# Optimization experiments

Measured on AMD Instinct MI355X. Metric: run time of the kernel, lower is better.

Reference implementation:

```python
import jax, jax.numpy as jnp
import numpy as np

N_M, N_D, N_A = 100000, 30000, 80000


def setup_inputs() -> dict:
    key = jax.random.key(0)
    ks = jax.random.split(key, 24)
    d_in, d_h, d_out = 64, 64, 32
    inp = {
        "x_movie": jax.random.normal(ks[0], (N_M, d_in), jnp.float32),
        "x_director": jax.random.normal(ks[1], (N_D, d_in), jnp.float32),
        "x_actor": jax.random.normal(ks[2], (N_A, d_in), jnp.float32),
        "src_md": jax.random.randint(ks[3], (1500000,), 0, N_M, jnp.int32),
        "dst_md": jax.random.randint(ks[4], (1500000,), 0, N_D, jnp.int32),
        "ew_md": jax.random.uniform(ks[5], (1500000,), jnp.float32),
        "src_dm": jax.random.randint(ks[6], (1500000,), 0, N_D, jnp.int32),
        "dst_dm": jax.random.randint(ks[7], (1500000,), 0, N_M, jnp.int32),
        "ew_dm": jax.random.uniform(ks[8], (1500000,), jnp.float32),
        "src_ma": jax.random.randint(ks[9], (2000000,), 0, N_M, jnp.int32),
        "dst_ma": jax.random.randint(ks[10], (2000000,), 0, N_A, jnp.int32),
        "ew_ma": jax.random.uniform(ks[11], (2000000,), jnp.float32),
        "src_am": jax.random.randint(ks[12], (2000000,), 0, N_A, jnp.int32),
        "dst_am": jax.random.randint(ks[13], (2000000,), 0, N_M, jnp.int32),
        "ew_am": jax.random.uniform(ks[14], (2000000,), jnp.float32),
        "W1_rel": jax.random.normal(ks[15], (4, d_in, d_h), jnp.float32) * 0.05,
        "b1": jax.random.normal(ks[16], (4, d_h), jnp.float32) * 0.05,
        "W1_root": jax.random.normal(ks[17], (4, d_in, d_h), jnp.float32) * 0.05,
        "W2_rel": jax.random.normal(ks[18], (4, d_h, d_out), jnp.float32) * 0.05,
        "b2": jax.random.normal(ks[19], (4, d_out), jnp.float32) * 0.05,
        "W2_root": jax.random.normal(ks[20], (4, d_h, d_out), jnp.float32) * 0.05,
    }
    return inp


def _hetero_layer(x_m, x_d, x_a, edges, ews, W_rel, b, W_root):
    # relation order: 0 = movie->director, 1 = director->movie,
    #                 2 = movie->actor,    3 = actor->movie
    (src_md, dst_md, src_dm, dst_dm, src_ma, dst_ma, src_am, dst_am) = edges
    (ew_md, ew_dm, ew_ma, ew_am) = ews
    # GraphConv: aggregate edge-weighted source features, then linear.
    agg_md = jax.ops.segment_sum(x_m[src_md] * ew_md[:, None], dst_md, num_segments=N_D)
    agg_dm = jax.ops.segment_sum(x_d[src_dm] * ew_dm[:, None], dst_dm, num_segments=N_M)
    agg_ma = jax.ops.segment_sum(x_m[src_ma] * ew_ma[:, None], dst_ma, num_segments=N_A)
    agg_am = jax.ops.segment_sum(x_a[src_am] * ew_am[:, None], dst_am, num_segments=N_M)
    out_d = agg_md @ W_rel[0] + b[0] + x_d @ W_root[0]
    out_m = (agg_dm @ W_rel[1] + b[1] + x_m @ W_root[1]) \
          + (agg_am @ W_rel[3] + b[3] + x_m @ W_root[3])  # HeteroConv aggr='sum'
    out_a = agg_ma @ W_rel[2] + b[2] + x_a @ W_root[2]
    return out_m, out_d, out_a


def reference(x_movie, x_director, x_actor,
              src_md, dst_md, ew_md, src_dm, dst_dm, ew_dm,
              src_ma, dst_ma, ew_ma, src_am, dst_am, ew_am,
              W1_rel, b1, W1_root, W2_rel, b2, W2_root):
    edges = (src_md, dst_md, src_dm, dst_dm, src_ma, dst_ma, src_am, dst_am)
    ews = (ew_md, ew_dm, ew_ma, ew_am)
    h_m, h_d, h_a = _hetero_layer(x_movie, x_director, x_actor, edges, ews, W1_rel, b1, W1_root)
    h_m, h_d, h_a = jax.nn.relu(h_m), jax.nn.relu(h_d), jax.nn.relu(h_a)
    o_m, o_d, o_a = _hetero_layer(h_m, h_d, h_a, edges, ews, W2_rel, b2, W2_root)
    return o_m, o_d, o_a
```

## Files before the change

### kernel.cpp

```cpp
#include <hip/hip_runtime.h>

#define N_M 100000
#define N_D 30000
#define N_A 80000

#define CSHIFT 14
#define NC_M 7
#define NC_D 2
#define NC_A 5

#define BO_MD 0
#define BO_DM (BO_MD + N_D * NC_M)
#define BO_MA (BO_DM + N_M * NC_D)
#define BO_AM (BO_MA + N_A * NC_M)
#define B_TOT (BO_AM + N_M * NC_A)

#define FBITS 12
#define NFINE 4096
#define NBUCK ((B_TOT + NFINE - 1) / NFINE)
#define T_A 4096

typedef unsigned int u32;
typedef unsigned short u16;
typedef unsigned long long u64;
// ... 150 lines not shown
    int gb = binBase0 + f0 + i;
    if (gb < B_TOT) bins[gb] = s0 + (int)ex;
    cur2[f0 + i] = ex;
    ex += v[i];
  }
  if (c == NBUCK - 1 && tid == 0) bins[B_TOT] = s1;
  __syncthreads();
  for (int e = s0 + tid; e < s1; e += 256) {
    u64 t = tmp[e];
    u32 fine = (u32)(t >> 32) & (NFINE - 1);
    u32 pos = atomicAdd(&cur2[fine], 1u);
    pairs[s0 + pos] = (u32)t;
  }
}

__global__ __launch_bounds__(256) void l1_tr_m(
    const float* __restrict__ x,
    const float* __restrict__ Wr0, const float* __restrict__ Wr2,
    const float* __restrict__ Wt1, const float* __restrict__ Wt3,
    const float* __restrict__ b1a, const float* __restrict__ b1b,
    u16* __restrict__ t0, u16* __restrict__ t2, u16* __restrict__ r, int n) {
  __shared__ float A[4096], B[4096], C[4096];
  for (int i = threadIdx.x * 4; i < 4096; i += 1024) {
    *(float4*)&A[i] = *(const float4*)&Wr0[i];
    *(float4*)&B[i] = *(const float4*)&Wr2[i];
    float4 p = *(const float4*)&Wt1[i], q = *(const float4*)&Wt3[i];
    *(float4*)&C[i] = make_float4(p.x + q.x, p.y + q.y, p.z + q.z, p.w + q.w);
  }
  __syncthreads();
  int lane = threadIdx.x & 63, wid = threadIdx.x >> 6;
  int wave = blockIdx.x * 4 + wid, nW = gridDim.x * 4;
  float bj = b1a[lane] + b1b[lane];
  for (int base = wave * 4; base < n; base += nW * 4) {
    int n0 = base, n1 = min(base + 1, n - 1), n2 = min(base + 2, n - 1), n3 = min(base + 3, n - 1);
    float o0a = 0, o0b = 0, o0c = bj, o1a = 0, o1b = 0, o1c = bj;
    float o2a = 0, o2b = 0, o2c = bj, o3a = 0, o3b = 0, o3c = bj;
#pragma unroll 4
    for (int k = 0; k < 64; k++) {
      float wa = A[k * 64 + lane], wb = B[k * 64 + lane], wc = C[k * 64 + lane];
      float x0 = x[(size_t)n0 * 64 + k], x1 = x[(size_t)n1 * 64 + k];
      float x2 = x[(size_t)n2 * 64 + k], x3 = x[(size_t)n3 * 64 + k];
      o0a = fmaf(x0, wa, o0a); o0b = fmaf(x0, wb, o0b); o0c = fmaf(x0, wc, o0c);
      o1a = fmaf(x1, wa, o1a); o1b = fmaf(x1, wb, o1b); o1c = fmaf(x1, wc, o1c);
      o2a = fmaf(x2, wa, o2a); o2b = fmaf(x2, wb, o2b); o2c = fmaf(x2, wc, o2c);
      o3a = fmaf(x3, wa, o3a); o3b = fmaf(x3, wb, o3b); o3c = fmaf(x3, wc, o3c);
    }
    t0[(size_t)n0 * 64 + lane] = f2bf(o0a); t2[(size_t)n0 * 64 + lane] = f2bf(o0b); r[(size_t)n0 * 64 + lane] = f2bf(o0c);
    if (base + 1 < n) { t0[(size_t)n1 * 64 + lane] = f2bf(o1a); t2[(size_t)n1 * 64 + lane] = f2bf(o1b); r[(size_t)n1 * 64 + lane] = f2bf(o1c); }
    if (base + 2 < n) { t0[(size_t)n2 * 64 + lane] = f2bf(o2a); t2[(size_t)n2 * 64 + lane] = f2bf(o2b); r[(size_t)n2 * 64 + lane] = f2bf(o2c); }
    if (base + 3 < n) { t0[(size_t)n3 * 64 + lane] = f2bf(o3a); t2[(size_t)n3 * 64 + lane] = f2bf(o3b); r[(size_t)n3 * 64 + lane] = f2bf(o3c); }
  }
}

__global__ __launch_bounds__(256) void l1_tr_s(
    const float* __restrict__ x,
    const float* __restrict__ Wrel, const float* __restrict__ Wroot,
    const float* __restrict__ bias,
    u16* __restrict__ t, u16* __restrict__ r, int n) {
  __shared__ float A[4096], C[4096];
  for (int i = threadIdx.x * 4; i < 4096; i += 1024) {
    *(float4*)&A[i] = *(const float4*)&Wrel[i];
    *(float4*)&C[i] = *(const float4*)&Wroot[i];
  }
  __syncthreads();
  int lane = threadIdx.x & 63, wid = threadIdx.x >> 6;
  int wave = blockIdx.x * 4 + wid, nW = gridDim.x * 4;
  float bj = bias[lane];
  for (int base = wave * 4; base < n; base += nW * 4) {
    int n0 = base, n1 = min(base + 1, n - 1), n2 = min(base + 2, n - 1), n3 = min(base + 3, n - 1);
    float o0a = 0, o0c = bj, o1a = 0, o1c = bj, o2a = 0, o2c = bj, o3a = 0, o3c = bj;
#pragma unroll 4
    for (int k = 0; k < 64; k++) {
      float wa = A[k * 64 + lane], wc = C[k * 64 + lane];
      float x0 = x[(size_t)n0 * 64 + k], x1 = x[(size_t)n1 * 64 + k];
      float x2 = x[(size_t)n2 * 64 + k], x3 = x[(size_t)n3 * 64 + k];
      o0a = fmaf(x0, wa, o0a); o0c = fmaf(x0, wc, o0c);
      o1a = fmaf(x1, wa, o1a); o1c = fmaf(x1, wc, o1c);
      o2a = fmaf(x2, wa, o2a); o2c = fmaf(x2, wc, o2c);
      o3a = fmaf(x3, wa, o3a); o3c = fmaf(x3, wc, o3c);
    }
    t[(size_t)n0 * 64 + lane] = f2bf(o0a); r[(size_t)n0 * 64 + lane] = f2bf(o0c);
    if (base + 1 < n) { t[(size_t)n1 * 64 + lane] = f2bf(o1a); r[(size_t)n1 * 64 + lane] = f2bf(o1c); }
    if (base + 2 < n) { t[(size_t)n2 * 64 + lane] = f2bf(o2a); r[(size_t)n2 * 64 + lane] = f2bf(o2c); }
    if (base + 3 < n) { t[(size_t)n3 * 64 + lane] = f2bf(o3a); r[(size_t)n3 * 64 + lane] = f2bf(o3c); }
  }
}

__device__ __forceinline__ void gather2_seg64(
    int s0, int s1, const u32* __restrict__ pairs,
    const u16* __restrict__ tbl, u32 lanebyte, u32 hm, int lane,
    float& a0, float& a1) {
  for (int base = s0; base < s1; base += 64) {
    int cnt = s1 - base; if (cnt > 64) cnt = 64;
    u32 pw = 0;
    if (base + lane < s1) pw = pairs[base + lane];
    int e = 0;
    for (; e + 4 <= cnt; e += 4) {
      u32 pa0 = __builtin_amdgcn_readlane(pw, e);
      u32 pb0 = __builtin_amdgcn_readlane(pw, e + 1);
      u32 pa1 = __builtin_amdgcn_readlane(pw, e + 2);
      u32 pb1 = __builtin_amdgcn_readlane(pw, e + 3);
      u32 offa0 = (pa0 >> 15) << 7;
      u32 offd0 = ((pb0 >> 15) << 7) - offa0;
      u32 wa0 = (pa0 & 0x7FFFu) << 16;
      u32 wd0 = (((pb0 & 0x7FFFu) << 16)) ^ wa0;
      u32 offa1 = (pa1 >> 15) << 7;
      u32 offd1 = ((pb1 >> 15) << 7) - offa1;
      u32 wa1 = (pa1 & 0x7FFFu) << 16;
      u32 wd1 = (((pb1 & 0x7FFFu) << 16)) ^ wa1;
      u32 off0 = (hm & offd0) + offa0 + lanebyte;
      u32 off1 = (hm & offd1) + offa1 + lanebyte;
      u32 v0 = *(const u32*)((const char*)tbl + off0);
      u32 v1 = *(const u32*)((const char*)tbl + off1);
      float w0 = __uint_as_float((hm & wd0) ^ wa0);
      float w1 = __uint_as_float((hm & wd1) ^ wa1);
      a0 = fmaf(w0, bf2f((u16)v0), a0);
      a1 = fmaf(w0, bf2f_hi(v0), a1);
      a0 = fmaf(w1, bf2f((u16)v1), a0);
      a1 = fmaf(w1, bf2f_hi(v1), a1);
    }
    if (e + 2 <= cnt) {
      u32 pa = __builtin_amdgcn_readlane(pw, e);
      u32 pb = __builtin_amdgcn_readlane(pw, e + 1);
      u32 offa = (pa >> 15) << 7;
      u32 offd = ((pb >> 15) << 7) - offa;
      u32 wa = (pa & 0x7FFFu) << 16;
      u32 wd = (((pb & 0x7FFFu) << 16)) ^ wa;
      u32 off = (hm & offd) + offa + lanebyte;
      u32 v = *(const u32*)((const char*)tbl + off);
      float w = __uint_as_float((hm & wd) ^ wa);
      a0 = fmaf(w, bf2f((u16)v), a0);
      a1 = fmaf(w, bf2f_hi(v), a1);
      e += 2;
    }
    if (e < cnt) {
      u32 p = __builtin_amdgcn_readlane(pw, e);
      u32 offa = (p >> 15) << 7;
      u32 wa = (p & 0x7FFFu) << 16;
      u32 off = offa + lanebyte;
      u32 v = *(const u32*)((const char*)tbl + off);
      float w = __uint_as_float((hm & wa) ^ wa);
      a0 = fmaf(w, bf2f((u16)v), a0);
      a1 = fmaf(w, bf2f_hi(v), a1);
    }
  }
}

__device__ __forceinline__ void gathero_32(
    int s0, int s1, const u32* __restrict__ pairs,
    const u16* __restrict__ ytbl, int lanebyte, int oaddr, int lane,
    float& a0, float& a1, float& a2, float& a3) {
  for (int base = s0; base < s1; base += 64) {
    u32 pw = 0;
    if (base + lane < s1) pw = pairs[base + lane];
    int ng = min(s1 - base, 64);
    ng = (ng + 7) >> 3;
#pragma unroll 2
    for (int g = 0; g < ng; g++) {
      u32 p = (u32)__builtin_amdgcn_ds_bpermute(oaddr + (g << 5), (int)pw);
      u32 off = ((p >> 15) << 6) + lanebyte;
      float w = __uint_as_float((p & 0x7FFFu) << 16);
      uint2 v = *(const uint2*)((const char*)ytbl + off);
      a0 = fmaf(w, bf2f((u16)v.x), a0);
      a1 = fmaf(w, bf2f_hi(v.x), a1);
      a2 = fmaf(w, bf2f((u16)v.y), a2);
      a3 = fmaf(w, bf2f_hi(v.y), a3);
    }
  }
}

__global__ __launch_bounds__(512) void fused1(
    const int* __restrict__ bins, const u32* __restrict__ pairs,
    const u16* __restrict__ tbl, const u16* __restrict__ r1,
    const float* __restrict__ W2r, const float* __restrict__ W2t,
    const float* __restrict__ b2s,
    u16* __restrict__ y, float* __restrict__ oroot,
    int n, int nC, int binBase) {
  __shared__ float Wy[2048], Wt[2048];
  __shared__ float bs[32];
  __shared__ __align__(16) float scr[8][64];
  for (int i = threadIdx.x; i < 2048; i += 512) { Wy[i] = W2r[i]; Wt[i] = W2t[i]; }
  if (threadIdx.x < 32) bs[threadIdx.x] = b2s[threadIdx.x];
  __syncthreads();
  int lane = threadIdx.x & 63, wid = threadIdx.x >> 6;
  int j = lane & 31, half = lane >> 5;
  u32 lanebyte = (u32)j << 2;
  u32 hm = half ? 0xFFFFFFFFu : 0u;
  int node0 = (blockIdx.x * 8 + wid) * 8;
  int bnd = bins[binBase + (node0 + min(lane, 8)) * nC];
  float acc0[8], acc1[8];
#pragma unroll
  for (int i = 0; i < 8; i++) { acc0[i] = 0.f; acc1[i] = 0.f; }
#pragma unroll
  for (int i = 0; i < 8; i++) {
    int s0 = __builtin_amdgcn_readlane(bnd, i);
    int s1 = __builtin_amdgcn_readlane(bnd, i + 1);
    if (node0 + i < n) gather2_seg64(s0, s1, pairs, tbl, lanebyte, hm, lane, acc0[i], acc1[i]);
  }
#pragma unroll
  for (int i = 0; i < 8; i++) {
    int node = node0 + i;
    if (node >= n) continue;
    float a0 = acc0[i] + __shfl_xor(acc0[i], 32);
    float a1 = acc1[i] + __shfl_xor(acc1[i], 32);
    u32 rv = *(const u32*)&r1[(size_t)node * 64 + 2 * j];
    float hv0 = fmaxf(a0 + bf2f((u16)rv), 0.f);
    float hv1 = fmaxf(a1 + bf2f_hi(rv), 0.f);
    if (!half) *(float2*)&scr[wid][2 * j] = make_float2(hv0, hv1);
    float oy = 0.f, ot = 0.f;
#pragma unroll
    for (int kk = 0; kk < 32; kk++) {
      int k = (half << 5) + kk;
      float s = scr[wid][k];
      oy = fmaf(s, Wy[k * 32 + j], oy);
      ot = fmaf(s, Wt[k * 32 + j], ot);
    }
    oy += __shfl_xor(oy, 32);
    ot += __shfl_xor(ot, 32);
    if (lane < 32) {
      y[(size_t)node * 32 + lane] = f2bf(oy);
      oroot[(size_t)node * 32 + lane] = ot + bs[lane];
    }
  }
}

__global__ __launch_bounds__(512) void fusedm(
    const int* __restrict__ bins, const u32* __restrict__ pairs,
    const u16* __restrict__ tbl1,
    const u16* __restrict__ tbl2,
    const u16* __restrict__ r1,
    const float* __restrict__ W2r0, const float* __restrict__ W2r2,
    const float* __restrict__ W2t1, const float* __restrict__ W2t3,
    const float* __restrict__ b2a, const float* __restrict__ b2b,
    u16* __restrict__ y0, u16* __restrict__ y2, float* __restrict__ oroot, int n) {
  __shared__ float Wy0[2048], Wy2[2048], Wt[2048];
  __shared__ float bs[32];
  __shared__ __align__(16) float scr[8][64];
  for (int i = threadIdx.x; i < 2048; i += 512) {
    Wy0[i] = W2r0[i]; Wy2[i] = W2r2[i]; Wt[i] = W2t1[i] + W2t3[i];
  }
  if (threadIdx.x < 32) bs[threadIdx.x] = b2a[threadIdx.x] + b2b[threadIdx.x];
  __syncthreads();
  int lane = threadIdx.x & 63, wid = threadIdx.x >> 6;
  int j = lane & 31, half = lane >> 5;
  u32 lanebyte = (u32)j << 2;
  u32 hm = half ? 0xFFFFFFFFu : 0u;
  int node0 = (blockIdx.x * 8 + wid) * 8;
  int bdm = bins[BO_DM + (node0 + min(lane, 8)) * NC_D];
  int bam = bins[BO_AM + (node0 + min(lane, 8)) * NC_A];
  float acc0[8], acc1[8];
#pragma unroll
  for (int i = 0; i < 8; i++) { acc0[i] = 0.f; acc1[i] = 0.f; }
#pragma unroll
  for (int i = 0; i < 8; i++) {
    int s0 = __builtin_amdgcn_readlane(bdm, i);
    int s1 = __builtin_amdgcn_readlane(bdm, i + 1);
    if (node0 + i < n) gather2_seg64(s0, s1, pairs, tbl1, lanebyte, hm, lane, acc0[i], acc1[i]);
  }
#pragma unroll
  for (int i = 0; i < 8; i++) {
    int s0 = __builtin_amdgcn_readlane(bam, i);
    int s1 = __builtin_amdgcn_readlane(bam, i + 1);
    if (node0 + i < n) gather2_seg64(s0, s1, pairs, tbl2, lanebyte, hm, lane, acc0[i], acc1[i]);
  }
#pragma unroll
  for (int i = 0; i < 8; i++) {
    int node = node0 + i;
    if (node >= n) continue;
    float a0 = acc0[i] + __shfl_xor(acc0[i], 32);
    float a1 = acc1[i] + __shfl_xor(acc1[i], 32);
    u32 rv = *(const u32*)&r1[(size_t)node * 64 + 2 * j];
    float hv0 = fmaxf(a0 + bf2f((u16)rv), 0.f);
    float hv1 = fmaxf(a1 + bf2f_hi(rv), 0.f);
    if (!half) *(float2*)&scr[wid][2 * j] = make_float2(hv0, hv1);
    float o0 = 0.f, o2 = 0.f, ot = 0.f;
#pragma unroll
    for (int kk = 0; kk < 32; kk++) {
      int k = (half << 5) + kk;
      float s = scr[wid][k];
      o0 = fmaf(s, Wy0[k * 32 + j], o0);
      o2 = fmaf(s, Wy2[k * 32 + j], o2);
      ot = fmaf(s, Wt[k * 32 + j], ot);
    }
    o0 += __shfl_xor(o0, 32);
    o2 += __shfl_xor(o2, 32);
    ot += __shfl_xor(ot, 32);
    if (lane < 32) {
      y0[(size_t)node * 32 + lane] = f2bf(o0);
      y2[(size_t)node * 32 + lane] = f2bf(o2);
      oroot[(size_t)node * 32 + lane] = ot + bs[lane];
    }
  }
}

__global__ __launch_bounds__(256) void out1(
    const int* __restrict__ bins, const u32* __restrict__ pairs,
    const u16* __restrict__ ytbl, float* __restrict__ out,
    int n, int nC, int binBase) {
  int lane = threadIdx.x & 63, wid = threadIdx.x >> 6;
  int node0 = (blockIdx.x * 4 + wid) * 8;
  int j8 = lane & 7;
  int lanebyte = j8 << 3;
  int oaddr = (lane >> 3) << 2;
  int bnd = bins[binBase + (node0 + min(lane, 8)) * nC];
  float acc0[8], acc1[8], acc2[8], acc3[8];
#pragma unroll
  for (int i = 0; i < 8; i++) { acc0[i] = 0.f; acc1[i] = 0.f; acc2[i] = 0.f; acc3[i] = 0.f; }
#pragma unroll
  for (int i = 0; i < 8; i++) {
    int s0 = __builtin_amdgcn_readlane(bnd, i);
    int s1 = __builtin_amdgcn_readlane(bnd, i + 1);
    if (node0 + i < n) gathero_32(s0, s1, pairs, ytbl, lanebyte, oaddr, lane,
                                  acc0[i], acc1[i], acc2[i], acc3[i]);
  }
#pragma unroll
  for (int i = 0; i < 8; i++) {
    int node = node0 + i;
    if (node >= n) continue;
    float a0 = acc0[i], a1 = acc1[i], a2 = acc2[i], a3 = acc3[i];
    a0 += __shfl_xor(a0, 8); a0 += __shfl_xor(a0, 16); a0 += __shfl_xor(a0, 32);
    a1 += __shfl_xor(a1, 8); a1 += __shfl_xor(a1, 16); a1 += __shfl_xor(a1, 32);
    a2 += __shfl_xor(a2, 8); a2 += __shfl_xor(a2, 16); a2 += __shfl_xor(a2, 32);
    a3 += __shfl_xor(a3, 8); a3 += __shfl_xor(a3, 16); a3 += __shfl_xor(a3, 32);
    if (lane < 8) {
      float4* o = (float4*)((char*)out + (size_t)node * 128 + (j8 << 4));
      float4 v = *o;
      v.x += a0; v.y += a1; v.z += a2; v.w += a3;
      *o = v;
    }
  }
}

__global__ __launch_bounds__(256) void outm(
    const int* __restrict__ bins, const u32* __restrict__ pairs,
    const u16* __restrict__ y1,
    const u16* __restrict__ y2,
    float* __restrict__ out, int n) {
  int lane = threadIdx.x & 63, wid = threadIdx.x >> 6;
  int node0 = (blockIdx.x * 4 + wid) * 8;
  int j8 = lane & 7;
  int lanebyte = j8 << 3;
  int oaddr = (lane >> 3) << 2;
  int bdm = bins[BO_DM + (node0 + min(lane, 8)) * NC_D];
  int bam = bins[BO_AM + (node0 + min(lane, 8)) * NC_A];
  float acc0[8], acc1[8], acc2[8], acc3[8];
#pragma unroll
  for (int i = 0; i < 8; i++) { acc0[i] = 0.f; acc1[i] = 0.f; acc2[i] = 0.f; acc3[i] = 0.f; }
#pragma unroll
  for (int i = 0; i < 8; i++) {
    int s0 = __builtin_amdgcn_readlane(bdm, i);
    int s1 = __builtin_amdgcn_readlane(bdm, i + 1);
    if (node0 + i < n) gathero_32(s0, s1, pairs, y1, lanebyte, oaddr, lane,
                                  acc0[i], acc1[i], acc2[i], acc3[i]);
  }
#pragma unroll
  for (int i = 0; i < 8; i++) {
    int s0 = __builtin_amdgcn_readlane(bam, i);
    int s1 = __builtin_amdgcn_readlane(bam, i + 1);
    if (node0 + i < n) gathero_32(s0, s1, pairs, y2, lanebyte, oaddr, lane,
                                  acc0[i], acc1[i], acc2[i], acc3[i]);
  }
#pragma unroll
  for (int i = 0; i < 8; i++) {
    int node = node0 + i;
    if (node >= n) continue;
    float a0 = acc0[i], a1 = acc1[i], a2 = acc2[i], a3 = acc3[i];
    a0 += __shfl_xor(a0, 8); a0 += __shfl_xor(a0, 16); a0 += __shfl_xor(a0, 32);
    a1 += __shfl_xor(a1, 8); a1 += __shfl_xor(a1, 16); a1 += __shfl_xor(a1, 32);
    a2 += __shfl_xor(a2, 8); a2 += __shfl_xor(a2, 16); a2 += __shfl_xor(a2, 32);
    a3 += __shfl_xor(a3, 8); a3 += __shfl_xor(a3, 16); a3 += __shfl_xor(a3, 32);
    if (lane < 8) {
      float4* o = (float4*)((char*)out + (size_t)node * 128 + (j8 << 4));
      float4 v = *o;
      v.x += a0; v.y += a1; v.z += a2; v.w += a3;
      *o = v;
    }
  }
}

static inline int nblkA(long long e) { return (int)((e + T_A - 1) / T_A); }

// ... 24 lines not shown

  const int E_md = in_sizes[3];
  const int E_dm = in_sizes[6];
  const int E_ma = in_sizes[9];
  const int E_am = in_sizes[12];
  const long long E_tot = (long long)E_md + E_dm + E_ma + E_am;

  char* w = (char*)d_ws;
  u64* tmp = (u64*)w;       w += (size_t)E_tot * 8;
  u32* pairs = (u32*)w;     w += (size_t)E_tot * 4;
  int* bins = (int*)w;      w += (size_t)(B_TOT + 1) * 4;
  int* bucketHist = (int*)w; w += 512 * 4;
  int* bucketBase = (int*)w; w += (NBUCK + 1) * 4;
  int* cursor = (int*)w;     w += 512 * 4;
  u16* r_d  = (u16*)w;      w += (size_t)N_D * 64 * 2;
  u16* r_a  = (u16*)w;      w += (size_t)N_A * 64 * 2;
  u16* y_md = (u16*)w;      w += (size_t)N_M * 32 * 2;
  u16* y_dm = (u16*)w;      w += (size_t)N_D * 32 * 2;
  u16* y_ma = (u16*)w;      w += (size_t)N_M * 32 * 2;
  u16* y_am = (u16*)w;      w += (size_t)N_A * 32 * 2;
  if ((size_t)(w - (char*)d_ws) > ws_size) return;
  char* ta = (char*)tmp;
  u16* t_md = (u16*)ta;     ta += (size_t)N_M * 64 * 2;
  u16* t_dm = (u16*)ta;     ta += (size_t)N_D * 64 * 2;
  u16* t_ma = (u16*)ta;     ta += (size_t)N_M * 64 * 2;
  u16* t_am = (u16*)ta;     ta += (size_t)N_A * 64 * 2;
  u16* r_m  = (u16*)ta;     ta += (size_t)N_M * 64 * 2;

  float* o_m = (float*)d_out;
  float* o_d = o_m + (size_t)N_M * 32;
  float* o_a = o_d + (size_t)N_D * 32;

  hipMemsetAsync(bucketHist, 0, 512 * 4, stream);

  Rel4 P;
  P.r[0] = { src_md, dst_md, ew_md, E_md, BO_MD, NC_M };
  P.r[1] = { src_dm, dst_dm, ew_dm, E_dm, BO_DM, NC_D };
  P.r[2] = { src_ma, dst_ma, ew_ma, E_ma, BO_MA, NC_M };
  P.r[3] = { src_am, dst_am, ew_am, E_am, BO_AM, NC_A };
  P.blkStart[0] = 0;
  P.blkStart[1] = P.blkStart[0] + nblkA(E_md);
  P.blkStart[2] = P.blkStart[1] + nblkA(E_dm);
  P.blkStart[3] = P.blkStart[2] + nblkA(E_ma);
  P.blkStart[4] = P.blkStart[3] + nblkA(E_am);

  phase0<<<P.blkStart[4], 256, 0, stream>>>(P, bucketHist);
  scan_bucket<<<1, 256, 0, stream>>>(bucketHist, bucketBase, cursor);
  phaseA<<<P.blkStart[4], 256, 0, stream>>>(P, cursor, tmp);
  phaseB<<<NBUCK, 256, 0, stream>>>(tmp, bucketBase, pairs, bins);

  l1_tr_m<<<768, 256, 0, stream>>>(x_m, W1_rel + 0 * 4096, W1_rel + 2 * 4096,
                                   W1_root + 1 * 4096, W1_root + 3 * 4096,
                                   b1 + 1 * 64, b1 + 3 * 64, t_md, t_ma, r_m, N_M);
  l1_tr_s<<<512, 256, 0, stream>>>(x_d, W1_rel + 1 * 4096, W1_root + 0 * 4096,
                                   b1 + 0 * 64, t_dm, r_d, N_D);
  l1_tr_s<<<512, 256, 0, stream>>>(x_a, W1_rel + 3 * 4096, W1_root + 2 * 4096,
                                   b1 + 2 * 64, t_am, r_a, N_A);

  fused1<<<(N_D + 63) / 64, 512, 0, stream>>>(bins, pairs, t_md, r_d,
      W2_rel + 1 * 2048, W2_root + 0 * 2048, b2 + 0 * 32, y_dm, o_d, N_D, NC_M, BO_MD);
  fused1<<<(N_A + 63) / 64, 512, 0, stream>>>(bins, pairs, t_ma, r_a,
      W2_rel + 3 * 2048, W2_root + 2 * 2048, b2 + 2 * 32, y_am, o_a, N_A, NC_M, BO_MA);
  fusedm<<<(N_M + 63) / 64, 512, 0, stream>>>(bins, pairs, t_dm, t_am, r_m,
      W2_rel + 0 * 2048, W2_rel + 2 * 2048, W2_root + 1 * 2048, W2_root + 3 * 2048,
      b2 + 1 * 32, b2 + 3 * 32, y_md, y_ma, o_m, N_M);

  out1<<<(N_D + 31) / 32, 256, 0, stream>>>(bins, pairs, y_md, o_d, N_D, NC_M, BO_MD);
  out1<<<(N_A + 31) / 32, 256, 0, stream>>>(bins, pairs, y_ma, o_a, N_A, NC_M, BO_MA);
  outm<<<(N_M + 31) / 32, 256, 0, stream>>>(bins, pairs, y_dm, y_am, o_m, N_M);
}
```

Baseline: 980.0 us.

## Fuse layer-2 director/actor output gather into fused1 by reordering after fusedm

```diff
diff --git a/kernel.cpp b/kernel.cpp
--- a/kernel.cpp
+++ b/kernel.cpp
@@ -257,6 +257,82 @@
     if (base + 1 < n) { t[(size_t)n1 * 64 + lane] = f2bf(o1a); r[(size_t)n1 * 64 + lane] = f2bf(o1c); }
     if (base + 2 < n) { t[(size_t)n2 * 64 + lane] = f2bf(o2a); r[(size_t)n2 * 64 + lane] = f2bf(o2c); }
     if (base + 3 < n) { t[(size_t)n3 * 64 + lane] = f2bf(o3a); r[(size_t)n3 * 64 + lane] = f2bf(o3c); }
+  }
+}
+
+__device__ __forceinline__ void gather2y_seg64(
+    int s0, int s1, const u32* __restrict__ pairs,
+    const u16* __restrict__ tbl, const u16* __restrict__ ytbl,
+    u32 lanebyte, u32 ylanebyte, u32 hm, int lane,
+    float& a0, float& a1, float& ay) {
+  for (int base = s0; base < s1; base += 64) {
+    int cnt = s1 - base; if (cnt > 64) cnt = 64;
+    u32 pw = 0;
+    if (base + lane < s1) pw = pairs[base + lane];
+    int e = 0;
+    for (; e + 4 <= cnt; e += 4) {
+      u32 pa0 = __builtin_amdgcn_readlane(pw, e);
+      u32 pb0 = __builtin_amdgcn_readlane(pw, e + 1);
+      u32 pa1 = __builtin_amdgcn_readlane(pw, e + 2);
+      u32 pb1 = __builtin_amdgcn_readlane(pw, e + 3);
+      u32 ra0 = pa0 >> 15, rb0 = pb0 >> 15;
+      u32 ra1 = pa1 >> 15, rb1 = pb1 >> 15;
+      u32 offa0 = ra0 << 7, offd0 = (rb0 << 7) - offa0;
+      u32 yoa0 = ra0 << 6,  yod0 = (rb0 << 6) - yoa0;
+      u32 wa0 = (pa0 & 0x7FFFu) << 16;
+      u32 wd0 = ((pb0 & 0x7FFFu) << 16) ^ wa0;
+      u32 offa1 = ra1 << 7, offd1 = (rb1 << 7) - offa1;
+      u32 yoa1 = ra1 << 6,  yod1 = (rb1 << 6) - yoa1;
+      u32 wa1 = (pa1 & 0x7FFFu) << 16;
+      u32 wd1 = ((pb1 & 0x7FFFu) << 16) ^ wa1;
+      u32 off0 = (hm & offd0) + offa0 + lanebyte;
+      u32 yof0 = (hm & yod0) + yoa0 + ylanebyte;
+      u32 off1 = (hm & offd1) + offa1 + lanebyte;
+      u32 yof1 = (hm & yod1) + yoa1 + ylanebyte;
+      u32 v0 = *(const u32*)((const char*)tbl + off0);
+      u16 q0 = *(const u16*)((const char*)ytbl + yof0);
+      u32 v1 = *(const u32*)((const char*)tbl + off1);
+      u16 q1 = *(const u16*)((const char*)ytbl + yof1);
+      float w0 = __uint_as_float((hm & wd0) ^ wa0);
+      float w1 = __uint_as_float((hm & wd1) ^ wa1);
+      a0 = fmaf(w0, bf2f((u16)v0), a0);
+      a1 = fmaf(w0, bf2f_hi(v0), a1);
+      ay = fmaf(w0, bf2f(q0), ay);
+      a0 = fmaf(w1, bf2f((u16)v1), a0);
+      a1 = fmaf(w1, bf2f_hi(v1), a1);
+      ay = fmaf(w1, bf2f(q1), ay);
+    }
+    if (e + 2 <= cnt) {
+      u32 pa = __builtin_amdgcn_readlane(pw, e);
+      u32 pb = __builtin_amdgcn_readlane(pw, e + 1);
+      u32 ra = pa >> 15, rb = pb >> 15;
+      u32 offa = ra << 7, offd = (rb << 7) - offa;
+      u32 yoa = ra << 6,  yod = (rb << 6) - yoa;
+      u32 wa = (pa & 0x7FFFu) << 16;
+      u32 wd = ((pb & 0x7FFFu) << 16) ^ wa;
+      u32 off = (hm & offd) + offa + lanebyte;
+      u32 yof = (hm & yod) + yoa + ylanebyte;
+      u32 v = *(const u32*)((const char*)tbl + off);
+      u16 q = *(const u16*)((const char*)ytbl + yof);
+      float w = __uint_as_float((hm & wd) ^ wa);
+      a0 = fmaf(w, bf2f((u16)v), a0);
+      a1 = fmaf(w, bf2f_hi(v), a1);
+      ay = fmaf(w, bf2f(q), ay);
+      e += 2;
+    }
+    if (e < cnt) {
+      u32 p = __builtin_amdgcn_readlane(pw, e);
+      u32 ra = p >> 15;
+      u32 wa = (p & 0x7FFFu) << 16;
+      u32 off = (ra << 7) + lanebyte;
+      u32 yof = (ra << 6) + ylanebyte;
+      u32 v = *(const u32*)((const char*)tbl + off);
+      u16 q = *(const u16*)((const char*)ytbl + yof);
+      float w = __uint_as_float((hm & wa) ^ wa);
+      a0 = fmaf(w, bf2f((u16)v), a0);
+      a1 = fmaf(w, bf2f_hi(v), a1);
+      ay = fmaf(w, bf2f(q), ay);
+    }
   }
 }
 
@@ -345,10 +421,11 @@
 
 __global__ __launch_bounds__(512) void fused1(
     const int* __restrict__ bins, const u32* __restrict__ pairs,
-    const u16* __restrict__ tbl, const u16* __restrict__ r1,
+    const u16* __restrict__ tbl, const u16* __restrict__ ytbl,
+    const u16* __restrict__ r1,
     const float* __restrict__ W2r, const float* __restrict__ W2t,
     const float* __restrict__ b2s,
-    u16* __restrict__ y, float* __restrict__ oroot,
+    u16* __restrict__ y, float* __restrict__ out,
     int n, int nC, int binBase) {
   __shared__ float Wy[2048], Wt[2048];
   __shared__ float bs[32];
@@ -359,17 +436,19 @@
   int lane = threadIdx.x & 63, wid = threadIdx.x >> 6;
   int j = lane & 31, half = lane >> 5;
   u32 lanebyte = (u32)j << 2;
+  u32 ylanebyte = (u32)j << 1;
   u32 hm = half ? 0xFFFFFFFFu : 0u;
   int node0 = (blockIdx.x * 8 + wid) * 8;
   int bnd = bins[binBase + (node0 + min(lane, 8)) * nC];
-  float acc0[8], acc1[8];
-#pragma unroll
-  for (int i = 0; i < 8; i++) { acc0[i] = 0.f; acc1[i] = 0.f; }
+  float acc0[8], acc1[8], accy[8];
+#pragma unroll
+  for (int i = 0; i < 8; i++) { acc0[i] = 0.f; acc1[i] = 0.f; accy[i] = 0.f; }
 #pragma unroll
   for (int i = 0; i < 8; i++) {
     int s0 = __builtin_amdgcn_readlane(bnd, i);
     int s1 = __builtin_amdgcn_readlane(bnd, i + 1);
-    if (node0 + i < n) gather2_seg64(s0, s1, pairs, tbl, lanebyte, hm, lane, acc0[i], acc1[i]);
+    if (node0 + i < n) gather2y_seg64(s0, s1, pairs, tbl, ytbl, lanebyte, ylanebyte, hm, lane,
+                                      acc0[i], acc1[i], accy[i]);
   }
 #pragma unroll
   for (int i = 0; i < 8; i++) {
@@ -377,6 +456,7 @@
     if (node >= n) continue;
     float a0 = acc0[i] + __shfl_xor(acc0[i], 32);
     float a1 = acc1[i] + __shfl_xor(acc1[i], 32);
+    float ayt = accy[i] + __shfl_xor(accy[i], 32);
     u32 rv = *(const u32*)&r1[(size_t)node * 64 + 2 * j];
     float hv0 = fmaxf(a0 + bf2f((u16)rv), 0.f);
     float hv1 = fmaxf(a1 + bf2f_hi(rv), 0.f);
@@ -393,7 +473,7 @@
     ot += __shfl_xor(ot, 32);
     if (lane < 32) {
       y[(size_t)node * 32 + lane] = f2bf(oy);
-      oroot[(size_t)node * 32 + lane] = ot + bs[lane];
+      out[(size_t)node * 32 + lane] = ot + bs[lane] + ayt;
     }
   }
 }
@@ -463,44 +543,6 @@
       y0[(size_t)node * 32 + lane] = f2bf(o0);
       y2[(size_t)node * 32 + lane] = f2bf(o2);
       oroot[(size_t)node * 32 + lane] = ot + bs[lane];
-    }
-  }
-}
-
-__global__ __launch_bounds__(256) void out1(
-    const int* __restrict__ bins, const u32* __restrict__ pairs,
-    const u16* __restrict__ ytbl, float* __restrict__ out,
-    int n, int nC, int binBase) {
-  int lane = threadIdx.x & 63, wid = threadIdx.x >> 6;
-  int node0 = (blockIdx.x * 4 + wid) * 8;
-  int j8 = lane & 7;
-  int lanebyte = j8 << 3;
-  int oaddr = (lane >> 3) << 2;
-  int bnd = bins[binBase + (node0 + min(lane, 8)) * nC];
-  float acc0[8], acc1[8], acc2[8], acc3[8];
-#pragma unroll
-  for (int i = 0; i < 8; i++) { acc0[i] = 0.f; acc1[i] = 0.f; acc2[i] = 0.f; acc3[i] = 0.f; }
-#pragma unroll
-  for (int i = 0; i < 8; i++) {
-    int s0 = __builtin_amdgcn_readlane(bnd, i);
-    int s1 = __builtin_amdgcn_readlane(bnd, i + 1);
-    if (node0 + i < n) gathero_32(s0, s1, pairs, ytbl, lanebyte, oaddr, lane,
-                                  acc0[i], acc1[i], acc2[i], acc3[i]);
-  }
-#pragma unroll
-  for (int i = 0; i < 8; i++) {
-    int node = node0 + i;
-    if (node >= n) continue;
-    float a0 = acc0[i], a1 = acc1[i], a2 = acc2[i], a3 = acc3[i];
-    a0 += __shfl_xor(a0, 8); a0 += __shfl_xor(a0, 16); a0 += __shfl_xor(a0, 32);
-    a1 += __shfl_xor(a1, 8); a1 += __shfl_xor(a1, 16); a1 += __shfl_xor(a1, 32);
-    a2 += __shfl_xor(a2, 8); a2 += __shfl_xor(a2, 16); a2 += __shfl_xor(a2, 32);
-    a3 += __shfl_xor(a3, 8); a3 += __shfl_xor(a3, 16); a3 += __shfl_xor(a3, 32);
-    if (lane < 8) {
-      float4* o = (float4*)((char*)out + (size_t)node * 128 + (j8 << 4));
-      float4 v = *o;
-      v.x += a0; v.y += a1; v.z += a2; v.w += a3;
-      *o = v;
     }
   }
 }
@@ -636,15 +678,14 @@
   l1_tr_s<<<512, 256, 0, stream>>>(x_a, W1_rel + 3 * 4096, W1_root + 2 * 4096,
                                    b1 + 2 * 64, t_am, r_a, N_A);
 
-  fused1<<<(N_D + 63) / 64, 512, 0, stream>>>(bins, pairs, t_md, r_d,
-      W2_rel + 1 * 2048, W2_root + 0 * 2048, b2 + 0 * 32, y_dm, o_d, N_D, NC_M, BO_MD);
-  fused1<<<(N_A + 63) / 64, 512, 0, stream>>>(bins, pairs, t_ma, r_a,
-      W2_rel + 3 * 2048, W2_root + 2 * 2048, b2 + 2 * 32, y_am, o_a, N_A, NC_M, BO_MA);
   fusedm<<<(N_M + 63) / 64, 512, 0, stream>>>(bins, pairs, t_dm, t_am, r_m,
       W2_rel + 0 * 2048, W2_rel + 2 * 2048, W2_root + 1 * 2048, W2_root + 3 * 2048,
       b2 + 1 * 32, b2 + 3 * 32, y_md, y_ma, o_m, N_M);
 
-  out1<<<(N_D + 31) / 32, 256, 0, stream>>>(bins, pairs, y_md, o_d, N_D, NC_M, BO_MD);
-  out1<<<(N_A + 31) / 32, 256, 0, stream>>>(bins, pairs, y_ma, o_a, N_A, NC_M, BO_MA);
+  fused1<<<(N_D + 63) / 64, 512, 0, stream>>>(bins, pairs, t_md, y_md, r_d,
+      W2_rel + 1 * 2048, W2_root + 0 * 2048, b2 + 0 * 32, y_dm, o_d, N_D, NC_M, BO_MD);
+  fused1<<<(N_A + 63) / 64, 512, 0, stream>>>(bins, pairs, t_ma, y_ma, r_a,
+      W2_rel + 3 * 2048, W2_root + 2 * 2048, b2 + 2 * 32, y_am, o_a, N_A, NC_M, BO_MA);
+
   outm<<<(N_M + 31) / 32, 256, 0, stream>>>(bins, pairs, y_dm, y_am, o_m, N_M);
 }
```

New measurement: 933.3 us. 4.8% less time.

## Fuse layer-2 director/actor output gather into fused1, merge launches, prefetch edge pairs

Applied to the files above, without the earlier changes.

```diff
diff --git a/kernel.cpp b/kernel.cpp
--- a/kernel.cpp
+++ b/kernel.cpp
@@ -226,97 +226,155 @@
   }
 }
 
-__global__ __launch_bounds__(256) void l1_tr_s(
-    const float* __restrict__ x,
-    const float* __restrict__ Wrel, const float* __restrict__ Wroot,
-    const float* __restrict__ bias,
-    u16* __restrict__ t, u16* __restrict__ r, int n) {
+__global__ __launch_bounds__(256) void l1_tr_s2(
+    const float* __restrict__ x1, const float* __restrict__ Wrel1,
+    const float* __restrict__ Wroot1, const float* __restrict__ bias1,
+    u16* __restrict__ t1o, u16* __restrict__ r1o, int n1, int nBlk1,
+    const float* __restrict__ x2, const float* __restrict__ Wrel2,
+    const float* __restrict__ Wroot2, const float* __restrict__ bias2,
+    u16* __restrict__ t2o, u16* __restrict__ r2o, int n2) {
   __shared__ float A[4096], C[4096];
+  bool first = (int)blockIdx.x < nBlk1;
+  const float* x = first ? x1 : x2;
+  const float* Wrel = first ? Wrel1 : Wrel2;
+  const float* Wroot = first ? Wroot1 : Wroot2;
+  const float* bias = first ? bias1 : bias2;
+  u16* t = first ? t1o : t2o;
+  u16* r = first ? r1o : r2o;
+  int n = first ? n1 : n2;
+  int blk = first ? blockIdx.x : blockIdx.x - nBlk1;
+  int nBlk = first ? nBlk1 : (gridDim.x - nBlk1);
   for (int i = threadIdx.x * 4; i < 4096; i += 1024) {
     *(float4*)&A[i] = *(const float4*)&Wrel[i];
     *(float4*)&C[i] = *(const float4*)&Wroot[i];
   }
   __syncthreads();
   int lane = threadIdx.x & 63, wid = threadIdx.x >> 6;
-  int wave = blockIdx.x * 4 + wid, nW = gridDim.x * 4;
+  int wave = blk * 4 + wid, nW = nBlk * 4;
   float bj = bias[lane];
   for (int base = wave * 4; base < n; base += nW * 4) {
-    int n0 = base, n1 = min(base + 1, n - 1), n2 = min(base + 2, n - 1), n3 = min(base + 3, n - 1);
+    int n0 = base, n1_ = min(base + 1, n - 1), n2_ = min(base + 2, n - 1), n3_ = min(base + 3, n - 1);
     float o0a = 0, o0c = bj, o1a = 0, o1c = bj, o2a = 0, o2c = bj, o3a = 0, o3c = bj;
 #pragma unroll 4
     for (int k = 0; k < 64; k++) {
       float wa = A[k * 64 + lane], wc = C[k * 64 + lane];
-      float x0 = x[(size_t)n0 * 64 + k], x1 = x[(size_t)n1 * 64 + k];
-      float x2 = x[(size_t)n2 * 64 + k], x3 = x[(size_t)n3 * 64 + k];
+      float x0 = x[(size_t)n0 * 64 + k], xx1 = x[(size_t)n1_ * 64 + k];
+      float xx2 = x[(size_t)n2_ * 64 + k], xx3 = x[(size_t)n3_ * 64 + k];
       o0a = fmaf(x0, wa, o0a); o0c = fmaf(x0, wc, o0c);
-      o1a = fmaf(x1, wa, o1a); o1c = fmaf(x1, wc, o1c);
-      o2a = fmaf(x2, wa, o2a); o2c = fmaf(x2, wc, o2c);
-      o3a = fmaf(x3, wa, o3a); o3c = fmaf(x3, wc, o3c);
+      o1a = fmaf(xx1, wa, o1a); o1c = fmaf(xx1, wc, o1c);
+      o2a = fmaf(xx2, wa, o2a); o2c = fmaf(xx2, wc, o2c);
+      o3a = fmaf(xx3, wa, o3a); o3c = fmaf(xx3, wc, o3c);
     }
     t[(size_t)n0 * 64 + lane] = f2bf(o0a); r[(size_t)n0 * 64 + lane] = f2bf(o0c);
-    if (base + 1 < n) { t[(size_t)n1 * 64 + lane] = f2bf(o1a); r[(size_t)n1 * 64 + lane] = f2bf(o1c); }
-    if (base + 2 < n) { t[(size_t)n2 * 64 + lane] = f2bf(o2a); r[(size_t)n2 * 64 + lane] = f2bf(o2c); }
-    if (base + 3 < n) { t[(size_t)n3 * 64 + lane] = f2bf(o3a); r[(size_t)n3 * 64 + lane] = f2bf(o3c); }
-  }
-}
+    if (base + 1 < n) { t[(size_t)n1_ * 64 + lane] = f2bf(o1a); r[(size_t)n1_ * 64 + lane] = f2bf(o1c); }
+    if (base + 2 < n) { t[(size_t)n2_ * 64 + lane] = f2bf(o2a); r[(size_t)n2_ * 64 + lane] = f2bf(o2c); }
+    if (base + 3 < n) { t[(size_t)n3_ * 64 + lane] = f2bf(o3a); r[(size_t)n3_ * 64 + lane] = f2bf(o3c); }
+  }
+}
+
+__device__ __forceinline__ void g2_pair(u32 pa, u32 pb,
+    const u16* __restrict__ tbl, u32 lanebyte, u32 hm,
+    float& a0, float& a1) {
+  u32 offa = (pa >> 15) << 7, offd = ((pb >> 15) << 7) - offa;
+  u32 wa = (pa & 0x7FFFu) << 16, wd = ((pb & 0x7FFFu) << 16) ^ wa;
+  u32 v = *(const u32*)((const char*)tbl + ((hm & offd) + offa + lanebyte));
+  float w = __uint_as_float((hm & wd) ^ wa);
+  a0 = fmaf(w, bf2f((u16)v), a0);
+  a1 = fmaf(w, bf2f_hi(v), a1);
+}
+
+__device__ __forceinline__ void g2y_pair(u32 pa, u32 pb,
+    const u16* __restrict__ tbl, const u16* __restrict__ ytbl,
+    u32 lanebyte, u32 ylanebyte, u32 hm,
+    float& a0, float& a1, float& ay) {
+  u32 ra = pa >> 15, rb = pb >> 15;
+  u32 offa = ra << 7, offd = (rb << 7) - offa;
+  u32 yoa = ra << 6,  yod = (rb << 6) - yoa;
+  u32 wa = (pa & 0x7FFFu) << 16, wd = ((pb & 0x7FFFu) << 16) ^ wa;
+  u32 v = *(const u32*)((const char*)tbl + ((hm & offd) + offa + lanebyte));
+  u16 q = *(const u16*)((const char*)ytbl + ((hm & yod) + yoa + ylanebyte));
+  float w = __uint_as_float((hm & wd) ^ wa);
+  a0 = fmaf(w, bf2f((u16)v), a0);
+  a1 = fmaf(w, bf2f_hi(v), a1);
+  ay = fmaf(w, bf2f(q), ay);
+}
+
+#define RL(x, i) ((u32)__builtin_amdgcn_readlane((int)(x), (i)))
 
 __device__ __forceinline__ void gather2_seg64(
     int s0, int s1, const u32* __restrict__ pairs,
-    const u16* __restrict__ tbl, u32 lanebyte, u32 hm, int lane,
+    const u16* __restrict__ tbl, u32 lanebyte, u32 hm, int lane, u32 pw0,
     float& a0, float& a1) {
-  for (int base = s0; base < s1; base += 64) {
+  int base = s0;
+  u32 pw = pw0;
+  for (;;) {
     int cnt = s1 - base; if (cnt > 64) cnt = 64;
-    u32 pw = 0;
-    if (base + lane < s1) pw = pairs[base + lane];
     int e = 0;
-    for (; e + 4 <= cnt; e += 4) {
-      u32 pa0 = __builtin_amdgcn_readlane(pw, e);
-      u32 pb0 = __builtin_amdgcn_readlane(pw, e + 1);
-      u32 pa1 = __builtin_amdgcn_readlane(pw, e + 2);
-      u32 pb1 = __builtin_amdgcn_readlane(pw, e + 3);
-      u32 offa0 = (pa0 >> 15) << 7;
-      u32 offd0 = ((pb0 >> 15) << 7) - offa0;
-      u32 wa0 = (pa0 & 0x7FFFu) << 16;
-      u32 wd0 = (((pb0 & 0x7FFFu) << 16)) ^ wa0;
-      u32 offa1 = (pa1 >> 15) << 7;
-      u32 offd1 = ((pb1 >> 15) << 7) - offa1;
-      u32 wa1 = (pa1 & 0x7FFFu) << 16;
-      u32 wd1 = (((pb1 & 0x7FFFu) << 16)) ^ wa1;
-      u32 off0 = (hm & offd0) + offa0 + lanebyte;
-      u32 off1 = (hm & offd1) + offa1 + lanebyte;
-      u32 v0 = *(const u32*)((const char*)tbl + off0);
-      u32 v1 = *(const u32*)((const char*)tbl + off1);
-      float w0 = __uint_as_float((hm & wd0) ^ wa0);
-      float w1 = __uint_as_float((hm & wd1) ^ wa1);
-      a0 = fmaf(w0, bf2f((u16)v0), a0);
-      a1 = fmaf(w0, bf2f_hi(v0), a1);
-      a0 = fmaf(w1, bf2f((u16)v1), a0);
-      a1 = fmaf(w1, bf2f_hi(v1), a1);
+    for (; e + 8 <= cnt; e += 8) {
+      u32 p0 = RL(pw, e),     p1 = RL(pw, e + 1), p2 = RL(pw, e + 2), p3 = RL(pw, e + 3);
+      u32 p4 = RL(pw, e + 4), p5 = RL(pw, e + 5), p6 = RL(pw, e + 6), p7 = RL(pw, e + 7);
+      g2_pair(p0, p1, tbl, lanebyte, hm, a0, a1);
+      g2_pair(p2, p3, tbl, lanebyte, hm, a0, a1);
+      g2_pair(p4, p5, tbl, lanebyte, hm, a0, a1);
+      g2_pair(p6, p7, tbl, lanebyte, hm, a0, a1);
+    }
+    if (e + 4 <= cnt) {
+      u32 p0 = RL(pw, e), p1 = RL(pw, e + 1), p2 = RL(pw, e + 2), p3 = RL(pw, e + 3);
+      g2_pair(p0, p1, tbl, lanebyte, hm, a0, a1);
+      g2_pair(p2, p3, tbl, lanebyte, hm, a0, a1);
+      e += 4;
     }
     if (e + 2 <= cnt) {
-      u32 pa = __builtin_amdgcn_readlane(pw, e);
-      u32 pb = __builtin_amdgcn_readlane(pw, e + 1);
-      u32 offa = (pa >> 15) << 7;
-      u32 offd = ((pb >> 15) << 7) - offa;
-      u32 wa = (pa & 0x7FFFu) << 16;
-      u32 wd = (((pb & 0x7FFFu) << 16)) ^ wa;
-      u32 off = (hm & offd) + offa + lanebyte;
-      u32 v = *(const u32*)((const char*)tbl + off);
-      float w = __uint_as_float((hm & wd) ^ wa);
-      a0 = fmaf(w, bf2f((u16)v), a0);
-      a1 = fmaf(w, bf2f_hi(v), a1);
+      u32 p0 = RL(pw, e), p1 = RL(pw, e + 1);
+      g2_pair(p0, p1, tbl, lanebyte, hm, a0, a1);
       e += 2;
     }
     if (e < cnt) {
-      u32 p = __builtin_amdgcn_readlane(pw, e);
-      u32 offa = (p >> 15) << 7;
-      u32 wa = (p & 0x7FFFu) << 16;
-      u32 off = offa + lanebyte;
-      u32 v = *(const u32*)((const char*)tbl + off);
-      float w = __uint_as_float((hm & wa) ^ wa);
-      a0 = fmaf(w, bf2f((u16)v), a0);
-      a1 = fmaf(w, bf2f_hi(v), a1);
-    }
+      u32 p = RL(pw, e);
+      g2_pair(p, p & 0xFFFF8000u, tbl, lanebyte, hm, a0, a1);
+    }
+    base += 64;
+    if (base >= s1) break;
+    pw = (base + lane < s1) ? pairs[base + lane] : 0u;
+  }
+}
+
+__device__ __forceinline__ void gather2y_seg64(
+    int s0, int s1, const u32* __restrict__ pairs,
+    const u16* __restrict__ tbl, const u16* __restrict__ ytbl,
+    u32 lanebyte, u32 ylanebyte, u32 hm, int lane, u32 pw0,
+    float& a0, float& a1, float& ay) {
+  int base = s0;
+  u32 pw = pw0;
+  for (;;) {
+    int cnt = s1 - base; if (cnt > 64) cnt = 64;
+    int e = 0;
+    for (; e + 8 <= cnt; e += 8) {
+      u32 p0 = RL(pw, e),     p1 = RL(pw, e + 1), p2 = RL(pw, e + 2), p3 = RL(pw, e + 3);
+      u32 p4 = RL(pw, e + 4), p5 = RL(pw, e + 5), p6 = RL(pw, e + 6), p7 = RL(pw, e + 7);
+      g2y_pair(p0, p1, tbl, ytbl, lanebyte, ylanebyte, hm, a0, a1, ay);
+      g2y_pair(p2, p3, tbl, ytbl, lanebyte, ylanebyte, hm, a0, a1, ay);
+      g2y_pair(p4, p5, tbl, ytbl, lanebyte, ylanebyte, hm, a0, a1, ay);
+      g2y_pair(p6, p7, tbl, ytbl, lanebyte, ylanebyte, hm, a0, a1, ay);
+    }
+    if (e + 4 <= cnt) {
+      u32 p0 = RL(pw, e), p1 = RL(pw, e + 1), p2 = RL(pw, e + 2), p3 = RL(pw, e + 3);
+      g2y_pair(p0, p1, tbl, ytbl, lanebyte, ylanebyte, hm, a0, a1, ay);
+      g2y_pair(p2, p3, tbl, ytbl, lanebyte, ylanebyte, hm, a0, a1, ay);
+      e += 4;
+    }
+    if (e + 2 <= cnt) {
+      u32 p0 = RL(pw, e), p1 = RL(pw, e + 1);
+      g2y_pair(p0, p1, tbl, ytbl, lanebyte, ylanebyte, hm, a0, a1, ay);
+      e += 2;
+    }
+    if (e < cnt) {
+      u32 p = RL(pw, e);
+      g2y_pair(p, p & 0xFFFF8000u, tbl, ytbl, lanebyte, ylanebyte, hm, a0, a1, ay);
+    }
+    base += 64;
+    if (base >= s1) break;
+    pw = (base + lane < s1) ? pairs[base + lane] : 0u;
   }
 }
 
@@ -343,41 +401,58 @@
   }
 }
 
+struct F1Side {
+  const u16 *tbl, *ytbl, *r1;
+  const float *W2r, *W2t, *b2;
+  u16 *y; float *out;
+  int n, nC, binBase;
+};
+
 __global__ __launch_bounds__(512) void fused1(
     const int* __restrict__ bins, const u32* __restrict__ pairs,
-    const u16* __restrict__ tbl, const u16* __restrict__ r1,
-    const float* __restrict__ W2r, const float* __restrict__ W2t,
-    const float* __restrict__ b2s,
-    u16* __restrict__ y, float* __restrict__ oroot,
-    int n, int nC, int binBase) {
+    F1Side D, F1Side A, int nBlkD) {
   __shared__ float Wy[2048], Wt[2048];
   __shared__ float bs[32];
   __shared__ __align__(16) float scr[8][64];
-  for (int i = threadIdx.x; i < 2048; i += 512) { Wy[i] = W2r[i]; Wt[i] = W2t[i]; }
-  if (threadIdx.x < 32) bs[threadIdx.x] = b2s[threadIdx.x];
+  bool isD = (int)blockIdx.x < nBlkD;
+  F1Side S = isD ? D : A;
+  int blk = isD ? blockIdx.x : blockIdx.x - nBlkD;
+  for (int i = threadIdx.x; i < 2048; i += 512) { Wy[i] = S.W2r[i]; Wt[i] = S.W2t[i]; }
+  if (threadIdx.x < 32) bs[threadIdx.x] = S.b2[threadIdx.x];
   __syncthreads();
   int lane = threadIdx.x & 63, wid = threadIdx.x >> 6;
   int j = lane & 31, half = lane >> 5;
   u32 lanebyte = (u32)j << 2;
+  u32 ylanebyte = (u32)j << 1;
   u32 hm = half ? 0xFFFFFFFFu : 0u;
-  int node0 = (blockIdx.x * 8 + wid) * 8;
-  int bnd = bins[binBase + (node0 + min(lane, 8)) * nC];
-  float acc0[8], acc1[8];
-#pragma unroll
-  for (int i = 0; i < 8; i++) { acc0[i] = 0.f; acc1[i] = 0.f; }
+  int node0 = (blk * 8 + wid) * 8;
+  int bnd = bins[S.binBase + (node0 + min(lane, 8)) * S.nC];
+  float acc0[8], acc1[8], accy[8];
+#pragma unroll
+  for (int i = 0; i < 8; i++) { acc0[i] = 0.f; acc1[i] = 0.f; accy[i] = 0.f; }
+  u32 pwp[8];
 #pragma unroll
   for (int i = 0; i < 8; i++) {
     int s0 = __builtin_amdgcn_readlane(bnd, i);
     int s1 = __builtin_amdgcn_readlane(bnd, i + 1);
-    if (node0 + i < n) gather2_seg64(s0, s1, pairs, tbl, lanebyte, hm, lane, acc0[i], acc1[i]);
+    pwp[i] = (node0 + i < S.n && s0 + lane < s1) ? pairs[s0 + lane] : 0u;
+  }
+#pragma unroll
+  for (int i = 0; i < 8; i++) {
+    int s0 = __builtin_amdgcn_readlane(bnd, i);
+    int s1 = __builtin_amdgcn_readlane(bnd, i + 1);
+    if (node0 + i < S.n)
+      gather2y_seg64(s0, s1, pairs, S.tbl, S.ytbl, lanebyte, ylanebyte, hm, lane, pwp[i],
+                     acc0[i], acc1[i], accy[i]);
   }
 #pragma unroll
   for (int i = 0; i < 8; i++) {
     int node = node0 + i;
-    if (node >= n) continue;
+    if (node >= S.n) continue;
     float a0 = acc0[i] + __shfl_xor(acc0[i], 32);
     float a1 = acc1[i] + __shfl_xor(acc1[i], 32);
-    u32 rv = *(const u32*)&r1[(size_t)node * 64 + 2 * j];
+    float ayt = accy[i] + __shfl_xor(accy[i], 32);
+    u32 rv = *(const u32*)&S.r1[(size_t)node * 64 + 2 * j];
     float hv0 = fmaxf(a0 + bf2f((u16)rv), 0.f);
     float hv1 = fmaxf(a1 + bf2f_hi(rv), 0.f);
     if (!half) *(float2*)&scr[wid][2 * j] = make_float2(hv0, hv1);
@@ -392,8 +467,8 @@
     oy += __shfl_xor(oy, 32);
     ot += __shfl_xor(ot, 32);
     if (lane < 32) {
-      y[(size_t)node * 32 + lane] = f2bf(oy);
-      oroot[(size_t)node * 32 + lane] = ot + bs[lane];
+      S.y[(size_t)node * 32 + lane] = f2bf(oy);
+      S.out[(size_t)node * 32 + lane] = ot + bs[lane] + ayt;
     }
   }
 }
@@ -425,17 +500,37 @@
   float acc0[8], acc1[8];
 #pragma unroll
   for (int i = 0; i < 8; i++) { acc0[i] = 0.f; acc1[i] = 0.f; }
-#pragma unroll
-  for (int i = 0; i < 8; i++) {
-    int s0 = __builtin_amdgcn_readlane(bdm, i);
-    int s1 = __builtin_amdgcn_readlane(bdm, i + 1);
-    if (node0 + i < n) gather2_seg64(s0, s1, pairs, tbl1, lanebyte, hm, lane, acc0[i], acc1[i]);
-  }
-#pragma unroll
-  for (int i = 0; i < 8; i++) {
-    int s0 = __builtin_amdgcn_readlane(bam, i);
-    int s1 = __builtin_amdgcn_readlane(bam, i + 1);
-    if (node0 + i < n) gather2_seg64(s0, s1, pairs, tbl2, lanebyte, hm, lane, acc0[i], acc1[i]);
+  {
+    u32 pwp[8];
+#pragma unroll
+    for (int i = 0; i < 8; i++) {
+      int s0 = __builtin_amdgcn_readlane(bdm, i);
+      int s1 = __builtin_amdgcn_readlane(bdm, i + 1);
+      pwp[i] = (node0 + i < n && s0 + lane < s1) ? pairs[s0 + lane] : 0u;
+    }
+#pragma unroll
+    for (int i = 0; i < 8; i++) {
+      int s0 = __builtin_amdgcn_readlane(bdm, i);
+      int s1 = __builtin_amdgcn_readlane(bdm, i + 1);
+      if (node0 + i < n)
+        gather2_seg64(s0, s1, pairs, tbl1, lanebyte, hm, lane, pwp[i], acc0[i], acc1[i]);
+    }
+  }
+  {
+    u32 pwp[8];
+#pragma unroll
+    for (int i = 0; i < 8; i++) {
+      int s0 = __builtin_amdgcn_readlane(bam, i);
+      int s1 = __builtin_amdgcn_readlane(bam, i + 1);
+      pwp[i] = (node0 + i < n && s0 + lane < s1) ? pairs[s0 + lane] : 0u;
+    }
+#pragma unroll
+    for (int i = 0; i < 8; i++) {
+      int s0 = __builtin_amdgcn_readlane(bam, i);
+      int s1 = __builtin_amdgcn_readlane(bam, i + 1);
+      if (node0 + i < n)
+        gather2_seg64(s0, s1, pairs, tbl2, lanebyte, hm, lane, pwp[i], acc0[i], acc1[i]);
+    }
   }
 #pragma unroll
   for (int i = 0; i < 8; i++) {
@@ -463,44 +558,6 @@
       y0[(size_t)node * 32 + lane] = f2bf(o0);
       y2[(size_t)node * 32 + lane] = f2bf(o2);
       oroot[(size_t)node * 32 + lane] = ot + bs[lane];
-    }
-  }
-}
-
-__global__ __launch_bounds__(256) void out1(
-    const int* __restrict__ bins, const u32* __restrict__ pairs,
-    const u16* __restrict__ ytbl, float* __restrict__ out,
-    int n, int nC, int binBase) {
-  int lane = threadIdx.x & 63, wid = threadIdx.x >> 6;
-  int node0 = (blockIdx.x * 4 + wid) * 8;
-  int j8 = lane & 7;
-  int lanebyte = j8 << 3;
-  int oaddr = (lane >> 3) << 2;
-  int bnd = bins[binBase + (node0 + min(lane, 8)) * nC];
-  float acc0[8], acc1[8], acc2[8], acc3[8];
-#pragma unroll
-  for (int i = 0; i < 8; i++) { acc0[i] = 0.f; acc1[i] = 0.f; acc2[i] = 0.f; acc3[i] = 0.f; }
-#pragma unroll
-  for (int i = 0; i < 8; i++) {
-    int s0 = __builtin_amdgcn_readlane(bnd, i);
-    int s1 = __builtin_amdgcn_readlane(bnd, i + 1);
-    if (node0 + i < n) gathero_32(s0, s1, pairs, ytbl, lanebyte, oaddr, lane,
-                                  acc0[i], acc1[i], acc2[i], acc3[i]);
-  }
-#pragma unroll
-  for (int i = 0; i < 8; i++) {
-    int node = node0 + i;
-    if (node >= n) continue;
-    float a0 = acc0[i], a1 = acc1[i], a2 = acc2[i], a3 = acc3[i];
-    a0 += __shfl_xor(a0, 8); a0 += __shfl_xor(a0, 16); a0 += __shfl_xor(a0, 32);
-    a1 += __shfl_xor(a1, 8); a1 += __shfl_xor(a1, 16); a1 += __shfl_xor(a1, 32);
-    a2 += __shfl_xor(a2, 8); a2 += __shfl_xor(a2, 16); a2 += __shfl_xor(a2, 32);
-    a3 += __shfl_xor(a3, 8); a3 += __shfl_xor(a3, 16); a3 += __shfl_xor(a3, 32);
-    if (lane < 8) {
-      float4* o = (float4*)((char*)out + (size_t)node * 128 + (j8 << 4));
-      float4 v = *o;
-      v.x += a0; v.y += a1; v.z += a2; v.w += a3;
-      *o = v;
     }
   }
 }
@@ -631,20 +688,21 @@
   l1_tr_m<<<768, 256, 0, stream>>>(x_m, W1_rel + 0 * 4096, W1_rel + 2 * 4096,
                                    W1_root + 1 * 4096, W1_root + 3 * 4096,
                                    b1 + 1 * 64, b1 + 3 * 64, t_md, t_ma, r_m, N_M);
-  l1_tr_s<<<512, 256, 0, stream>>>(x_d, W1_rel + 1 * 4096, W1_root + 0 * 4096,
-                                   b1 + 0 * 64, t_dm, r_d, N_D);
-  l1_tr_s<<<512, 256, 0, stream>>>(x_a, W1_rel + 3 * 4096, W1_root + 2 * 4096,
-                                   b1 + 2 * 64, t_am, r_a, N_A);
-
-  fused1<<<(N_D + 63) / 64, 512, 0, stream>>>(bins, pairs, t_md, r_d,
-      W2_rel + 1 * 2048, W2_root + 0 * 2048, b2 + 0 * 32, y_dm, o_d, N_D, NC_M, BO_MD);
-  fused1<<<(N_A + 63) / 64, 512, 0, stream>>>(bins, pairs, t_ma, r_a,
-      W2_rel + 3 * 2048, W2_root + 2 * 2048, b2 + 2 * 32, y_am, o_a, N_A, NC_M, BO_MA);
+  l1_tr_s2<<<1024, 256, 0, stream>>>(
+      x_d, W1_rel + 1 * 4096, W1_root + 0 * 4096, b1 + 0 * 64, t_dm, r_d, N_D, 512,
+      x_a, W1_rel + 3 * 4096, W1_root + 2 * 4096, b1 + 2 * 64, t_am, r_a, N_A);
+
   fusedm<<<(N_M + 63) / 64, 512, 0, stream>>>(bins, pairs, t_dm, t_am, r_m,
       W2_rel + 0 * 2048, W2_rel + 2 * 2048, W2_root + 1 * 2048, W2_root + 3 * 2048,
       b2 + 1 * 32, b2 + 3 * 32, y_md, y_ma, o_m, N_M);
 
-  out1<<<(N_D + 31) / 32, 256, 0, stream>>>(bins, pairs, y_md, o_d, N_D, NC_M, BO_MD);
-  out1<<<(N_A + 31) / 32, 256, 0, stream>>>(bins, pairs, y_ma, o_a, N_A, NC_M, BO_MA);
+  int nBlkD = (N_D + 63) / 64;
+  int nBlkA_ = (N_A + 63) / 64;
+  F1Side Dside = { t_md, y_md, r_d, W2_rel + 1 * 2048, W2_root + 0 * 2048, b2 + 0 * 32,
+                   y_dm, o_d, N_D, NC_M, BO_MD };
+  F1Side Aside = { t_ma, y_ma, r_a, W2_rel + 3 * 2048, W2_root + 2 * 2048, b2 + 2 * 32,
+                   y_am, o_a, N_A, NC_M, BO_MA };
+  fused1<<<nBlkD + nBlkA_, 512, 0, stream>>>(bins, pairs, Dside, Aside, nBlkD);
+
   outm<<<(N_M + 31) / 32, 256, 0, stream>>>(bins, pairs, y_dm, y_am, o_m, N_M);
 }
```

After: 875.2 us. -10.7%, faster.
